# Kernel optimization log

Hardware: AMD Instinct MI355X
Metric: run time of the kernel (lower is better)

## Reference

```python
import jax, jax.numpy as jnp
import numpy as np

B, S, E, A = 4, 4096, 512, 64

def setup_inputs() -> dict:
    key = jax.random.key(0)
    ks = jax.random.split(key, 9)
    return {
        "query": jax.random.normal(ks[0], (B, S, E), dtype=jnp.float32),
        "key":   jax.random.normal(ks[1], (B, S, E), dtype=jnp.float32),
        "value": jax.random.normal(ks[2], (B, S, E), dtype=jnp.float32),
        "Wq": jax.random.normal(ks[3], (E, A), dtype=jnp.float32) / np.sqrt(E),
        "bq": jax.random.normal(ks[4], (A,), dtype=jnp.float32) * 0.01,
        "Wk": jax.random.normal(ks[5], (E, A), dtype=jnp.float32) / np.sqrt(E),
        "bk": jax.random.normal(ks[6], (A,), dtype=jnp.float32) * 0.01,
        "Wv": jax.random.normal(ks[7], (E, A), dtype=jnp.float32) / np.sqrt(E),
        "bv": jax.random.normal(ks[8], (A,), dtype=jnp.float32) * 0.01,
        "look_ahead_mask": 1,
    }

def reference(query, key, value, Wq, bq, Wk, bk, Wv, bv, look_ahead_mask):
    # Linear projections (torch Linear: x @ W^T + b; here W stored as [in,out])
    q = query @ Wq + bq            # [B,S,A]
    k = key   @ Wk + bk            # [B,S,A]
    v = value @ Wv + bv            # [B,S,A]
    scale = jnp.sqrt(jnp.asarray(A, dtype=q.dtype))
    qk = jnp.einsum('bsa,bta->bst', q, k) / scale   # [B,S,S]
    if look_ahead_mask:
        # faithful to source: MULTIPLICATIVE tril mask (not additive -inf)
        tril = jnp.tril(jnp.ones((qk.shape[-1], qk.shape[-1]), dtype=qk.dtype))
        qk = qk * tril
    attn = jax.nn.softmax(qk, axis=-1)              # [B,S,S]
    return jnp.einsum('bst,bta->bsa', attn, v)       # [B,S,A]
```

## Files before the change

### kernel.cpp

```cpp
#include <hip/hip_runtime.h>
#include <cstdint>

constexpr int BB = 4, SS = 4096, EE = 512, AA = 64;
constexpr int NT = 64;
constexpr int NSL = 288;

typedef __bf16 bf16x8 __attribute__((ext_vector_type(8)));
typedef float  f32x4  __attribute__((ext_vector_type(4)));
typedef float  f4     __attribute__((ext_vector_type(4)));
typedef unsigned short u16x4 __attribute__((ext_vector_type(4)));
typedef unsigned short u16x8 __attribute__((ext_vector_type(8)));

#define MFMA16(a, b, c) __builtin_amdgcn_mfma_f32_16x16x32_bf16((a), (b), (c), 0, 0, 0)

typedef const void __attribute__((address_space(1))) gvoid_t;
typedef void __attribute__((address_space(3))) lvoid_t;
__device__ __forceinline__ void gload16(const void* g, void* l) {
    __builtin_amdgcn_global_load_lds((gvoid_t*)g, (lvoid_t*)l, 16, 0, 0);
}

__device__ __forceinline__ unsigned short f2bf(float x) {
    union { float f; unsigned u; } v; v.f = x;
    unsigned r = v.u + 0x7fffu + ((v.u >> 16) & 1u);
    return (unsigned short)(r >> 16);
}
__device__ __forceinline__ float bf2f(unsigned short h) {
    union { unsigned u; float f; } v; v.u = ((unsigned)h) << 16;
    return v.f;
}
__device__ __forceinline__ bf16x8 as_bf16x8(u16x8 u) {
    union { u16x8 u; bf16x8 b; } v; v.u = u; return v.b;
}

__global__ void split_w_kernel(const float* __restrict__ Wq,
                               const float* __restrict__ Wk,
                               const float* __restrict__ Wv,
                               unsigned short* __restrict__ wt_h,
                               unsigned short* __restrict__ wt_l) {
    int idx = blockIdx.x * blockDim.x + threadIdx.x;
    if (idx >= 3 * EE * AA) return;
    int t = idx / (EE * AA);
    int rem = idx - t * (EE * AA);
    int k = rem >> 6;
    int n = rem & 63;
    const float* W = (t == 0) ? Wq : (t == 1) ? Wk : Wv;
    float x = W[k * AA + n];
    unsigned short h = f2bf(x);
    unsigned short l = f2bf(x - bf2f(h));
    int o = (t * AA + n) * EE + k;
    wt_h[o] = h;
    wt_l[o] = l;
}

__launch_bounds__(256)
__global__ void proj_kernel(const float* __restrict__ Xq,
                            const float* __restrict__ Xk,
                            const float* __restrict__ Xv,
                            const float* __restrict__ bq,
                            const float* __restrict__ bk,
                            const float* __restrict__ bv,
                            const unsigned short* __restrict__ wt_h,
                            const unsigned short* __restrict__ wt_l,
                            unsigned short* __restrict__ q_hi,
                            unsigned short* __restrict__ q_lo,
                            unsigned short* __restrict__ kv) {
    const int t = blockIdx.y;
    const float* X    = (t == 0) ? Xq : (t == 1) ? Xk : Xv;
    const float* bias = (t == 0) ? bq : (t == 1) ? bk : bv;
    const int row0 = blockIdx.x * 64;
    const int tid = threadIdx.x;
    const int lane = tid & 63, w = tid >> 6;
    const int l15 = lane & 15, l4 = lane >> 4;

    __shared__ __align__(16) char smem[32768];

    f32x4 acc[4];
#pragma unroll
    for (int j = 0; j < 4; ++j) acc[j] = (f32x4){0.f, 0.f, 0.f, 0.f};

    const unsigned short* wtH = wt_h + t * AA * EE;
    const unsigned short* wtL = wt_l + t * AA * EE;

    for (int kc0 = 0; kc0 < EE; kc0 += 64) {
#pragma unroll
        for (int s = 0; s < 4; ++s) {
            int r = w * 16 + s * 4 + (lane >> 4);
            int c4 = (lane & 15) ^ (r & 7);
            gload16(X + (size_t)(row0 + r) * EE + kc0 + c4 * 4,
                    smem + w * 4096 + s * 1024 + lane * 16);
        }
#pragma unroll
        for (int s = 0; s < 2; ++s) {
            int n = w * 16 + s * 8 + (lane >> 3);
            int cg = (lane & 7) ^ (n & 7);
            gload16(wtH + n * EE + kc0 + cg * 8,
                    smem + 16384 + w * 2048 + s * 1024 + lane * 16);
            gload16(wtL + n * EE + kc0 + cg * 8,
                    smem + 24576 + w * 2048 + s * 1024 + lane * 16);
        }
        asm volatile("s_waitcnt vmcnt(0)" ::: "memory");
        __syncthreads();

#pragma unroll
        for (int kc = 0; kc < 2; ++kc) {
            int r = w * 16 + l15;
            int c4a = (kc * 8 + l4 * 2) ^ (r & 7);
            int c4b = (kc * 8 + l4 * 2 + 1) ^ (r & 7);
            f4 va = *(const f4*)(smem + r * 256 + c4a * 16);
            f4 vb = *(const f4*)(smem + r * 256 + c4b * 16);
            u16x8 ahu, alu;
#pragma unroll
            for (int jj = 0; jj < 4; ++jj) {
                unsigned short h0 = f2bf(va[jj]);
                ahu[jj] = h0;
                alu[jj] = f2bf(va[jj] - bf2f(h0));
                unsigned short h1 = f2bf(vb[jj]);
                ahu[jj + 4] = h1;
                alu[jj + 4] = f2bf(vb[jj] - bf2f(h1));
            }
            bf16x8 a_h = as_bf16x8(ahu), a_l = as_bf16x8(alu);
#pragma unroll
            for (int j = 0; j < 4; ++j) {
                int n = j * 16 + l15;
                int byteB = n * 128 + (((kc * 4 + l4) ^ (n & 7)) << 4);
                bf16x8 b_h = as_bf16x8(*(const u16x8*)(smem + 16384 + byteB));
                bf16x8 b_l = as_bf16x8(*(const u16x8*)(smem + 24576 + byteB));
                acc[j] = MFMA16(a_h, b_h, acc[j]);
                acc[j] = MFMA16(a_h, b_l, acc[j]);
                acc[j] = MFMA16(a_l, b_h, acc[j]);
            }
        }
        __syncthreads();
    }

    float* stage = (float*)smem;
#pragma unroll
    for (int j = 0; j < 4; ++j) {
        int n = j * 16 + l15;
        float bv_ = bias[n];
#pragma unroll
        for (int reg = 0; reg < 4; ++reg) {
            int r = w * 16 + l4 * 4 + reg;
            stage[r * 65 + n] = acc[j][reg] + bv_;
        }
    }
    __syncthreads();

    if (t == 0) {
        int row = tid >> 2, n0 = (tid & 3) * 16;
        u16x8 h0, l0, h1, l1;
#pragma unroll
        for (int k = 0; k < 8; ++k) {
            float v = stage[row * 65 + n0 + k];
            unsigned short hh = f2bf(v);
            h0[k] = hh; l0[k] = f2bf(v - bf2f(hh));
        }
#pragma unroll
        for (int k = 0; k < 8; ++k) {
            float v = stage[row * 65 + n0 + 8 + k];
            unsigned short hh = f2bf(v);
            h1[k] = hh; l1[k] = f2bf(v - bf2f(hh));
        }
        size_t o = (size_t)(row0 + row) * AA + n0;
        *(u16x8*)(q_hi + o) = h0; *(u16x8*)(q_hi + o + 8) = h1;
        *(u16x8*)(q_lo + o) = l0; *(u16x8*)(q_lo + o + 8) = l1;
    } else {
        const int bb = row0 >> 12, kt = (row0 & 4095) >> 6;
        const size_t base = ((size_t)(bb * NT + kt) << 14) + (t == 2 ? 8192 : 0);
        const int f = tid >> 5;
#pragma unroll
        for (int p = 0; p < 2; ++p) {
            int lane2 = (tid & 31) * 2 + p;
            u16x8 h, l;
            if (t == 1) {
                int n0 = (f >> 2) * 32 + (lane2 >> 4) * 8;
                int tt = (f & 3) * 16 + (lane2 & 15);
#pragma unroll
                for (int jj = 0; jj < 8; ++jj) {
                    float v = stage[tt * 65 + n0 + jj];
                    unsigned short hh = f2bf(v);
                    h[jj] = hh; l[jj] = f2bf(v - bf2f(hh));
                }
            } else {
                int tt0 = (f >> 2) * 32 + (lane2 >> 4) * 8;
                int n = (f & 3) * 16 + (lane2 & 15);
#pragma unroll
                for (int jj = 0; jj < 8; ++jj) {
                    float v = stage[(tt0 + jj) * 65 + n];
                    unsigned short hh = f2bf(v);
                    h[jj] = hh; l[jj] = f2bf(v - bf2f(hh));
                }
            }
            size_t o = base + f * 512 + lane2 * 8;
            *(u16x8*)(kv + o) = h;
            *(u16x8*)(kv + o + 4096) = l;
        }
    }
}

__launch_bounds__(64)
__global__ void sufv_kernel(const unsigned short* __restrict__ kv,
                            float* __restrict__ sufv) {
    const int b = blockIdx.x >> 6;
    const int a = blockIdx.x & 63;
    const int t = threadIdx.x;
    __shared__ float sums[64];
    const size_t tb = ((size_t)(b * NT + t) << 14) + 8192;
    const int j = a >> 4, l15i = a & 15;
    float s = 0.f;
#pragma unroll
    for (int c2 = 0; c2 < 2; ++c2) {
#pragma unroll
        for (int l4i = 0; l4i < 4; ++l4i) {
            size_t off = tb + (((c2 * 4 + j) * 64 + l4i * 16 + l15i) << 3);
            u16x8 h = *(const u16x8*)(kv + off);
            u16x8 l = *(const u16x8*)(kv + off + 4096);
#pragma unroll
            for (int q = 0; q < 8; ++q) s += bf2f(h[q]) + bf2f(l[q]);
        }
    }
    sums[t] = s;
    __syncthreads();
    float suf = 0.f;
    for (int jj = t + 1; jj < 64; ++jj) suf += sums[jj];
    sufv[((size_t)(b * 64 + a)) * 64 + t] = suf;
}

__launch_bounds__(256)
__global__ void attn_chunk_kernel(const unsigned short* __restrict__ q_hi,
                                  const unsigned short* __restrict__ q_lo,
                                  const unsigned short* __restrict__ kv,
                                  float* __restrict__ facc_part,
                                  float* __restrict__ l_part) {
    const int bxr = (NSL - 1) - blockIdx.x;
    const int b = blockIdx.y;
    int g = 7;
    while (4 * g * (g + 1) > bxr) --g;
    const int r_ = bxr - 4 * g * (g + 1);
    const int q_ = (int)((float)r_ * (1.0f / (float)(g + 1)) + 1e-4f);
    const int i  = g * 8 + q_;
    const int c  = r_ - q_ * (g + 1);
    const int t_begin = c * 8;
    const int t_end   = (t_begin + 8 < i + 1) ? t_begin + 8 : i + 1;

    const int tid = threadIdx.x;
    const int lane = tid & 63, w = tid >> 6;
    const int l15 = lane & 15, l4 = lane >> 4;

    __shared__ __align__(16) unsigned short kvbuf[16384];
    __shared__ __align__(16) unsigned short plds[4][1024];

    bf16x8 qh[2], ql[2];
    {
        size_t qrow = (size_t)(b * SS + i * 64 + w * 16 + l15) * AA;
#pragma unroll
        for (int kc = 0; kc < 2; ++kc) {
            qh[kc] = as_bf16x8(*(const u16x8*)(q_hi + qrow + kc * 32 + l4 * 8));
            ql[kc] = as_bf16x8(*(const u16x8*)(q_lo + qrow + kc * 32 + l4 * 8));
        }
    }

    f32x4 facc[4];
#pragma unroll
    for (int j = 0; j < 4; ++j) facc[j] = (f32x4){0.f, 0.f, 0.f, 0.f};
    float lsum = 0.f;

    const char* gbase_p = (const char*)kv + (((size_t)(b * NT)) << 15) +
                          w * 8192 + lane * 16;
    char* lw = (char*)kvbuf + w * 8192 + lane * 16;
    const char* lb = (const char*)kvbuf;

    f4 rr[8];

    {
        const char* gt = gbase_p + (((size_t)t_begin) << 15);
#pragma unroll
        for (int s = 0; s < 8; ++s) rr[s] = *(const f4*)(gt + s * 1024);
#pragma unroll
        for (int s = 0; s < 8; ++s) *(f4*)(lw + s * 1024) = rr[s];
    }
    __syncthreads();

    for (int kt = t_begin; kt < t_end; ++kt) {
        const bool more = (kt + 1 < t_end);
        if (more) {
            const char* gt = gbase_p + (((size_t)(kt + 1)) << 15);
#pragma unroll
            for (int s = 0; s < 8; ++s) rr[s] = *(const f4*)(gt + s * 1024);
        }
        __builtin_amdgcn_sched_barrier(0);

        f32x4 sc[4];
#pragma unroll
        for (int j = 0; j < 4; ++j) sc[j] = (f32x4){0.f, 0.f, 0.f, 0.f};
        __builtin_amdgcn_s_setprio(1);
#pragma unroll
        for (int kc = 0; kc < 2; ++kc) {
#pragma unroll
            for (int j2 = 0; j2 < 4; ++j2) {
                int f = kc * 4 + j2;
                bf16x8 h = as_bf16x8(*(const u16x8*)(lb + f * 1024 + lane * 16));
                bf16x8 l = as_bf16x8(*(const u16x8*)(lb + 8192 + f * 1024 + lane * 16));
                sc[j2] = MFMA16(h, qh[kc], sc[j2]);
                sc[j2] = MFMA16(l, qh[kc], sc[j2]);
                sc[j2] = MFMA16(h, ql[kc], sc[j2]);
            }
        }
        __builtin_amdgcn_s_setprio(0);

        const bool diag = (kt == i);
#pragma unroll
        for (int j2 = 0; j2 < 4; ++j2) {
            u16x4 p4;
#pragma unroll
            for (int reg = 0; reg < 4; ++reg) {
                float s = sc[j2][reg] * 0.125f;
                if (diag) {
                    int qr = w * 16 + l15;
                    int tg = j2 * 16 + l4 * 4 + reg;
                    if (tg > qr) s = 0.f;
                }
                float p = __expf(s);
                lsum += p;
                p4[reg] = f2bf(p);
            }
            int byte = (l15 * 128 + j2 * 32 + l4 * 8) ^ ((l15 & 7) << 4);
            *(u16x4*)((char*)plds[w] + byte) = p4;
        }

        __builtin_amdgcn_s_setprio(1);
#pragma unroll
        for (int c2 = 0; c2 < 2; ++c2) {
            int byteA = (l15 * 128 + c2 * 64 + l4 * 16) ^ ((l15 & 7) << 4);
            bf16x8 pf = as_bf16x8(*(const u16x8*)((const char*)plds[w] + byteA));
#pragma unroll
            for (int j = 0; j < 4; ++j) {
                int f = c2 * 4 + j;
                bf16x8 vh = as_bf16x8(*(const u16x8*)(lb + 16384 + f * 1024 + lane * 16));
                bf16x8 vl = as_bf16x8(*(const u16x8*)(lb + 24576 + f * 1024 + lane * 16));
                facc[j] = MFMA16(pf, vh, facc[j]);
                facc[j] = MFMA16(pf, vl, facc[j]);
            }
        }
        __builtin_amdgcn_s_setprio(0);

        if (more) {
            __syncthreads();
#pragma unroll
            for (int s = 0; s < 8; ++s) *(f4*)(lw + s * 1024) = rr[s];
            __syncthreads();
        }
    }

    {
        float rs = lsum;
        rs += __shfl_xor(rs, 16);
        rs += __shfl_xor(rs, 32);
        const size_t slot = (size_t)b * NSL + bxr;
        if (l4 == 0)
            l_part[slot * 64 + w * 16 + l15] = rs;

        float* fp = facc_part + slot * 4096;
#pragma unroll
        for (int j = 0; j < 4; ++j) {
#pragma unroll
            for (int reg = 0; reg < 4; ++reg) {
                int row = w * 16 + l4 * 4 + reg, a = j * 16 + l15;
                fp[row * 64 + a] = facc[j][reg];
            }
        }
    }
}

__launch_bounds__(256)
__global__ void combine_kernel(const float* __restrict__ facc_part,
                               const float* __restrict__ l_part,
                               const float* __restrict__ sufv,
                               float* __restrict__ out) {
    const int i = blockIdx.x;
    const int b = blockIdx.y;
    const int tid = threadIdx.x;
    const int g = i >> 3;
    const int nch = g + 1;
    const size_t slot0 = (size_t)b * NSL + 4 * g * (g + 1) + (i & 7) * nch;
    __shared__ float linv[64];
    __shared__ float sv[64];
    if (tid < 64) {
        float l = (float)(64 * (NT - 1 - i));
        for (int cc = 0; cc < nch; ++cc) l += l_part[(slot0 + cc) * 64 + tid];
        linv[tid] = 1.f / l;
        sv[tid] = sufv[((size_t)(b * 64 + tid)) * 64 + i];
    }
    __syncthreads();
    float* ob = out + ((size_t)(b * SS + i * 64)) * AA;
#pragma unroll
    for (int k = 0; k < 4; ++k) {
        int e = (tid + k * 256) * 4;
        int row = e >> 6, a = e & 63;
        f4 acc = {sv[a], sv[a + 1], sv[a + 2], sv[a + 3]};
        for (int cc = 0; cc < nch; ++cc) {
            f4 v = *(const f4*)(facc_part + (slot0 + cc) * 4096 + e);
            acc += v;
        }
        acc *= linv[row];
        *(f4*)(ob + e) = acc;
    }
}

extern "C" void kernel_launch(void* const* d_in, const int* in_sizes, int n_in,
                              void* d_out, int out_size, void* d_ws, size_t ws_size,
                              hipStream_t stream) {
    const float* query = (const float*)d_in[0];
    const float* key   = (const float*)d_in[1];
    const float* value = (const float*)d_in[2];
    const float* Wq    = (const float*)d_in[3];
    const float* bq    = (const float*)d_in[4];
    const float* Wk    = (const float*)d_in[5];
    const float* bk    = (const float*)d_in[6];
    const float* Wv    = (const float*)d_in[7];
    const float* bv    = (const float*)d_in[8];

    char* ws = (char*)d_ws;
    const size_t MB = 1u << 20;
    unsigned short* q_hi = (unsigned short*)(ws + 0 * MB);
    unsigned short* q_lo = (unsigned short*)(ws + 2 * MB);
    unsigned short* kv   = (unsigned short*)(ws + 4 * MB);
    float* sufv      = (float*)(ws + 12 * MB);
    float* l_part    = (float*)(ws + 13 * MB);
    float* facc_part = (float*)(ws + 14 * MB);
    unsigned short* wt_h = (unsigned short*)(ws + 34 * MB);
    unsigned short* wt_l = wt_h + 3 * AA * EE;

    split_w_kernel<<<(3 * EE * AA + 255) / 256, 256, 0, stream>>>(Wq, Wk, Wv, wt_h, wt_l);
    proj_kernel<<<dim3(BB * SS / 64, 3), 256, 0, stream>>>(
        query, key, value, bq, bk, bv, wt_h, wt_l, q_hi, q_lo, kv);
    sufv_kernel<<<BB * AA, 64, 0, stream>>>(kv, sufv);
    attn_chunk_kernel<<<dim3(NSL, BB), 256, 0, stream>>>(
        q_hi, q_lo, kv, facc_part, l_part);
    combine_kernel<<<dim3(NT, BB), 256, 0, stream>>>(facc_part, l_part, sufv, (float*)d_out);
}
```

Baseline: 90.32 us.

## Use 128-row query tiles with 512-thread blocks and direct-to-LDS KV loads

The attention chunk kernel now handles 128 query rows per block across 8 waves instead of 64 rows across 4, so every KV tile staged in LDS serves twice as many queries and the slot count is halved. The register-staged prefetch is replaced by global_load_lds transfers followed by a full wait, which removes the overlap between loading and compute. The 1/sqrt(A) scale is folded into Q during projection, and the causal mask now uses a per-row offset test. The combine kernel is adjusted to read the new 128-row partial layout.

```diff
diff --git a/kernel.cpp b/kernel.cpp
--- a/kernel.cpp
+++ b/kernel.cpp
@@ -3,7 +3,7 @@
 
 constexpr int BB = 4, SS = 4096, EE = 512, AA = 64;
 constexpr int NT = 64;
-constexpr int NSL = 288;
+constexpr int NSLOT = 144;
 
 typedef __bf16 bf16x8 __attribute__((ext_vector_type(8)));
 typedef float  f32x4  __attribute__((ext_vector_type(4)));
@@ -151,13 +151,13 @@
         u16x8 h0, l0, h1, l1;
 #pragma unroll
         for (int k = 0; k < 8; ++k) {
-            float v = stage[row * 65 + n0 + k];
+            float v = stage[row * 65 + n0 + k] * 0.125f;
             unsigned short hh = f2bf(v);
             h0[k] = hh; l0[k] = f2bf(v - bf2f(hh));
         }
 #pragma unroll
         for (int k = 0; k < 8; ++k) {
-            float v = stage[row * 65 + n0 + 8 + k];
+            float v = stage[row * 65 + n0 + 8 + k] * 0.125f;
             unsigned short hh = f2bf(v);
             h1[k] = hh; l1[k] = f2bf(v - bf2f(hh));
         }
@@ -226,33 +226,34 @@
     sufv[((size_t)(b * 64 + a)) * 64 + t] = suf;
 }
 
-__launch_bounds__(256)
+__launch_bounds__(512)
 __global__ void attn_chunk_kernel(const unsigned short* __restrict__ q_hi,
                                   const unsigned short* __restrict__ q_lo,
                                   const unsigned short* __restrict__ kv,
                                   float* __restrict__ facc_part,
                                   float* __restrict__ l_part) {
-    const int bxr = (NSL - 1) - blockIdx.x;
+    const int s = (NSLOT - 1) - blockIdx.x;
     const int b = blockIdx.y;
-    int g = 7;
-    while (4 * g * (g + 1) > bxr) --g;
-    const int r_ = bxr - 4 * g * (g + 1);
-    const int q_ = (int)((float)r_ * (1.0f / (float)(g + 1)) + 1e-4f);
-    const int i  = g * 8 + q_;
-    const int c  = r_ - q_ * (g + 1);
+    int m = 7;
+    while (2 * m * (m + 1) > s) --m;
+    const int rem = s - 2 * m * (m + 1);
+    const int r_ = rem / (m + 1);
+    const int c  = rem - r_ * (m + 1);
+    const int i  = 4 * m + r_;
     const int t_begin = c * 8;
-    const int t_end   = (t_begin + 8 < i + 1) ? t_begin + 8 : i + 1;
+    const int tmax = 2 * i + 2;
+    const int t_end = (t_begin + 8 < tmax) ? t_begin + 8 : tmax;
 
     const int tid = threadIdx.x;
     const int lane = tid & 63, w = tid >> 6;
     const int l15 = lane & 15, l4 = lane >> 4;
 
     __shared__ __align__(16) unsigned short kvbuf[16384];
-    __shared__ __align__(16) unsigned short plds[4][1024];
+    __shared__ __align__(16) unsigned short plds[8][1024];
 
     bf16x8 qh[2], ql[2];
     {
-        size_t qrow = (size_t)(b * SS + i * 64 + w * 16 + l15) * AA;
+        size_t qrow = (size_t)(b * SS + i * 128 + w * 16 + l15) * AA;
 #pragma unroll
         for (int kc = 0; kc < 2; ++kc) {
             qh[kc] = as_bf16x8(*(const u16x8*)(q_hi + qrow + kc * 32 + l4 * 8));
@@ -265,30 +266,18 @@
     for (int j = 0; j < 4; ++j) facc[j] = (f32x4){0.f, 0.f, 0.f, 0.f};
     float lsum = 0.f;
 
-    const char* gbase_p = (const char*)kv + (((size_t)(b * NT)) << 15) +
-                          w * 8192 + lane * 16;
-    char* lw = (char*)kvbuf + w * 8192 + lane * 16;
     const char* lb = (const char*)kvbuf;
-
-    f4 rr[8];
-
-    {
-        const char* gt = gbase_p + (((size_t)t_begin) << 15);
-#pragma unroll
-        for (int s = 0; s < 8; ++s) rr[s] = *(const f4*)(gt + s * 1024);
-#pragma unroll
-        for (int s = 0; s < 8; ++s) *(f4*)(lw + s * 1024) = rr[s];
-    }
-    __syncthreads();
+    const int qbase = i * 128 + w * 16;
 
     for (int kt = t_begin; kt < t_end; ++kt) {
-        const bool more = (kt + 1 < t_end);
-        if (more) {
-            const char* gt = gbase_p + (((size_t)(kt + 1)) << 15);
-#pragma unroll
-            for (int s = 0; s < 8; ++s) rr[s] = *(const f4*)(gt + s * 1024);
-        }
-        __builtin_amdgcn_sched_barrier(0);
+        {
+            const char* gt = (const char*)kv + (((size_t)(b * NT + kt)) << 15) + tid * 16;
+            char* lw = (char*)kvbuf + tid * 16;
+#pragma unroll
+            for (int p = 0; p < 4; ++p) gload16(gt + p * 8192, lw + p * 8192);
+        }
+        asm volatile("s_waitcnt vmcnt(0)" ::: "memory");
+        __syncthreads();
 
         f32x4 sc[4];
 #pragma unroll
@@ -308,19 +297,19 @@
         }
         __builtin_amdgcn_s_setprio(0);
 
-        const bool diag = (kt == i);
+        const int dq = qbase - 64 * kt;
+        const bool anyMask = (dq < 63);
 #pragma unroll
         for (int j2 = 0; j2 < 4; ++j2) {
             u16x4 p4;
 #pragma unroll
             for (int reg = 0; reg < 4; ++reg) {
-                float s = sc[j2][reg] * 0.125f;
-                if (diag) {
-                    int qr = w * 16 + l15;
-                    int tg = j2 * 16 + l4 * 4 + reg;
-                    if (tg > qr) s = 0.f;
+                float sv_ = sc[j2][reg];
+                if (anyMask) {
+                    int tl = j2 * 16 + l4 * 4 + reg;
+                    if (tl > dq + l15) sv_ = 0.f;
                 }
-                float p = __expf(s);
+                float p = __expf(sv_);
                 lsum += p;
                 p4[reg] = f2bf(p);
             }
@@ -344,23 +333,18 @@
         }
         __builtin_amdgcn_s_setprio(0);
 
-        if (more) {
-            __syncthreads();
-#pragma unroll
-            for (int s = 0; s < 8; ++s) *(f4*)(lw + s * 1024) = rr[s];
-            __syncthreads();
-        }
+        if (kt + 1 < t_end) __syncthreads();
     }
 
     {
         float rs = lsum;
         rs += __shfl_xor(rs, 16);
         rs += __shfl_xor(rs, 32);
-        const size_t slot = (size_t)b * NSL + bxr;
+        const size_t slot = (size_t)b * NSLOT + s;
         if (l4 == 0)
-            l_part[slot * 64 + w * 16 + l15] = rs;
-
-        float* fp = facc_part + slot * 4096;
+            l_part[slot * 128 + w * 16 + l15] = rs;
+
+        float* fp = facc_part + slot * 8192;
 #pragma unroll
         for (int j = 0; j < 4; ++j) {
 #pragma unroll
@@ -377,29 +361,32 @@
                                const float* __restrict__ l_part,
                                const float* __restrict__ sufv,
                                float* __restrict__ out) {
-    const int i = blockIdx.x;
+    const int i64 = blockIdx.x;
     const int b = blockIdx.y;
     const int tid = threadIdx.x;
-    const int g = i >> 3;
-    const int nch = g + 1;
-    const size_t slot0 = (size_t)b * NSL + 4 * g * (g + 1) + (i & 7) * nch;
+    const int i128 = i64 >> 1;
+    const int m = i128 >> 2;
+    const int nch = m + 1;
+    const size_t slot0 = (size_t)b * NSLOT + 2 * m * (m + 1) + (i128 & 3) * nch;
+    const int rbase = (i64 & 1) * 64;
     __shared__ float linv[64];
     __shared__ float sv[64];
     if (tid < 64) {
-        float l = (float)(64 * (NT - 1 - i));
-        for (int cc = 0; cc < nch; ++cc) l += l_part[(slot0 + cc) * 64 + tid];
+        float l = 64.0f * (float)(NT - 2 * i128 - 2);
+        for (int cc = 0; cc < nch; ++cc)
+            l += l_part[(slot0 + cc) * 128 + rbase + tid];
         linv[tid] = 1.f / l;
-        sv[tid] = sufv[((size_t)(b * 64 + tid)) * 64 + i];
+        sv[tid] = sufv[((size_t)(b * 64 + tid)) * 64 + (2 * i128 + 1)];
     }
     __syncthreads();
-    float* ob = out + ((size_t)(b * SS + i * 64)) * AA;
+    float* ob = out + ((size_t)(b * SS + i64 * 64)) * AA;
 #pragma unroll
     for (int k = 0; k < 4; ++k) {
         int e = (tid + k * 256) * 4;
         int row = e >> 6, a = e & 63;
         f4 acc = {sv[a], sv[a + 1], sv[a + 2], sv[a + 3]};
         for (int cc = 0; cc < nch; ++cc) {
-            f4 v = *(const f4*)(facc_part + (slot0 + cc) * 4096 + e);
+            f4 v = *(const f4*)(facc_part + (slot0 + cc) * 8192 + (rbase + row) * 64 + a);
             acc += v;
         }
         acc *= linv[row];
@@ -435,7 +422,7 @@
     proj_kernel<<<dim3(BB * SS / 64, 3), 256, 0, stream>>>(
         query, key, value, bq, bk, bv, wt_h, wt_l, q_hi, q_lo, kv);
     sufv_kernel<<<BB * AA, 64, 0, stream>>>(kv, sufv);
-    attn_chunk_kernel<<<dim3(NSL, BB), 256, 0, stream>>>(
+    attn_chunk_kernel<<<dim3(NSLOT, BB), 512, 0, stream>>>(
         q_hi, q_lo, kv, facc_part, l_part);
     combine_kernel<<<dim3(NT, BB), 256, 0, stream>>>(facc_part, l_part, sufv, (float*)d_out);
 }
```

Measured after the change: 90.75 us. No clear change (+0.5%).
